# Kernel optimization log

Measured on AMD Instinct MI355X. Metric: run time of the kernel, lower is better.

The kernel has to match this reference:

```python
import jax, jax.numpy as jnp
import numpy as np

B, T, D_IN, H, D_OUT = 64, 512, 256, 1024, 256


def _gru_cell(x, h, Wi, Wh, bi, bh):
    # x: [B, in_dim], h: [B, H]; Wi: [3H, in_dim], Wh: [3H, H]
    gi = x @ Wi.T + bi  # [B, 3H]
    gh = h @ Wh.T + bh  # [B, 3H]
    i_r, i_z, i_n = jnp.split(gi, 3, axis=-1)
    h_r, h_z, h_n = jnp.split(gh, 3, axis=-1)
    r = jax.nn.sigmoid(i_r + h_r)
    z = jax.nn.sigmoid(i_z + h_z)
    n = jnp.tanh(i_n + r * h_n)
    return (1.0 - z) * n + z * h


def setup_inputs() -> dict:
    key = jax.random.key(0)
    ks = jax.random.split(key, 11)
    s_in = 1.0 / np.sqrt(D_IN)
    s_h = 1.0 / np.sqrt(H)
    return {
        "x": jax.random.normal(ks[0], (B, T, D_IN), jnp.float32),
        "Wi0": jax.random.normal(ks[1], (3 * H, D_IN), jnp.float32) * s_in,
        "Wh0": jax.random.normal(ks[2], (3 * H, H), jnp.float32) * s_h,
        "bi0": jax.random.normal(ks[3], (3 * H,), jnp.float32) * s_h,
        "bh0": jax.random.normal(ks[4], (3 * H,), jnp.float32) * s_h,
        "Wi1": jax.random.normal(ks[5], (3 * H, H), jnp.float32) * s_h,
        "Wh1": jax.random.normal(ks[6], (3 * H, H), jnp.float32) * s_h,
        "bi1": jax.random.normal(ks[7], (3 * H,), jnp.float32) * s_h,
        "bh1": jax.random.normal(ks[8], (3 * H,), jnp.float32) * s_h,
        "Wo": jax.random.normal(ks[9], (D_OUT, H), jnp.float32) * s_h,
        "bo": jax.random.normal(ks[10], (D_OUT,), jnp.float32) * s_h,
    }


def reference(x, Wi0, Wh0, bi0, bh0, Wi1, Wh1, bi1, bh1, Wo, bo):
    b = x.shape[0]
    h0 = jnp.zeros((b, H), x.dtype)
    h1 = jnp.zeros((b, H), x.dtype)

    def step(carry, x_t):
        h0, h1 = carry
        h0 = _gru_cell(x_t, h0, Wi0, Wh0, bi0, bh0)
        h1 = _gru_cell(h0, h1, Wi1, Wh1, bi1, bh1)
        return (h0, h1), None

    (h0, h1), _ = jax.lax.scan(step, (h0, h1), jnp.swapaxes(x, 0, 1))
    return h1 @ Wo.T + bo  # [B, D_OUT]
```

## Files before the change

### kernel.cpp

```cpp
#include <hip/hip_runtime.h>

constexpr int kB    = 64;
constexpr int kT    = 512;
constexpr int kDin  = 256;
constexpr int kH    = 1024;
constexpr int kH3   = 3072;
constexpr int kDout = 256;
constexpr int kHB   = kB * kH;

typedef float  f32x4  __attribute__((ext_vector_type(4)));
typedef __bf16 bf16x8 __attribute__((ext_vector_type(8)));
typedef unsigned u32x4 __attribute__((ext_vector_type(4)));
typedef unsigned long long u64;

__device__ __forceinline__ float b2f(unsigned short u) {
  union { float f; unsigned u32; } c; c.u32 = ((unsigned)u) << 16; return c.f;
}
__device__ __forceinline__ unsigned short f2b(float f) {
  union { float f; unsigned u32; } c; c.f = f;
  unsigned r = c.u32 + 0x7fffu + ((c.u32 >> 16) & 1u);
  return (unsigned short)(r >> 16);
}
__device__ __forceinline__ bf16x8 ld8(const unsigned short* p) {
  return *reinterpret_cast<const bf16x8*>(p);
}
__device__ __forceinline__ u64 ald(const u64* p) {
  return __hip_atomic_load(p, __ATOMIC_RELAXED, __HIP_MEMORY_SCOPE_AGENT);
}
__device__ __forceinline__ unsigned ald32(const unsigned* p) {
  return __hip_atomic_load(p, __ATOMIC_RELAXED, __HIP_MEMORY_SCOPE_AGENT);
}
__device__ __forceinline__ void ast32(unsigned* p, unsigned v) {
  __hip_atomic_store(p, v, __ATOMIC_RELAXED, __HIP_MEMORY_SCOPE_AGENT);
}
__device__ __forceinline__ float sigm_(float x) { return 1.f / (1.f + __expf(-x)); }
__device__ __forceinline__ float tanh_(float x) {
  return 1.f - 2.f / (__expf(2.f * x) + 1.f);
}

#define MFMA16(a, b, c) __builtin_amdgcn_mfma_f32_16x16x32_bf16((a), (b), (c), 0, 0, 0)

__device__ __forceinline__ int swzcol(int C, int quad) {
  return (C & ~63) + ((quad ^ (((C >> 3) ^ (C >> 6)) & 7)) << 3);
}

__global__ void gru_prep(const float* __restrict__ x,
                         const float* __restrict__ Wi0, const float* __restrict__ Wh0,
                         const float* __restrict__ bi0, const float* __restrict__ bh0,
                         const float* __restrict__ Wi1, const float* __restrict__ Wh1,
                         const float* __restrict__ bi1, const float* __restrict__ bh1,
                         unsigned short* __restrict__ xb,
                         unsigned short* __restrict__ wi0b, unsigned short* __restrict__ wh0b,
                         unsigned short* __restrict__ wi1b, unsigned short* __restrict__ wh1b,
                         unsigned short* __restrict__ r0, unsigned short* __restrict__ r1,
                         float* __restrict__ bias, unsigned* __restrict__ sync) {
  const int stride = gridDim.x * blockDim.x;
  const int g = blockIdx.x * blockDim.x + threadIdx.x;
  for (int i = g; i < kH3 * kDin; i += stride) wi0b[i] = f2b(Wi0[i]);
  for (int i = g; i < kH3 * kH; i += stride) {
    wh0b[i] = f2b(Wh0[i]); wi1b[i] = f2b(Wi1[i]); wh1b[i] = f2b(Wh1[i]);
  }
  for (int i = g; i < kB * kT * kDin; i += stride) xb[i] = f2b(x[i]);
  for (int i = g; i < kHB; i += stride) { r0[i] = 0; r1[i] = 0; }
  for (int i = g; i < kH; i += stride) {
    bias[0 * kH + i] = bi0[0 * kH + i] + bh0[0 * kH + i];
    bias[1 * kH + i] = bi0[1 * kH + i] + bh0[1 * kH + i];
    bias[2 * kH + i] = bi0[2 * kH + i];
    bias[3 * kH + i] = bh0[2 * kH + i];
    bias[4 * kH + i] = bi1[0 * kH + i] + bh1[0 * kH + i];
    bias[5 * kH + i] = bi1[1 * kH + i] + bh1[1 * kH + i];
    bias[6 * kH + i] = bi1[2 * kH + i];
    bias[7 * kH + i] = bh1[2 * kH + i];
  }
  for (int i = g; i < 1024; i += stride) sync[i] = 0;
}

__global__ void __launch_bounds__(256, 1) gru_main(
    const unsigned short* __restrict__ xb,
    const unsigned short* __restrict__ wi0, const unsigned short* __restrict__ wh0,
    const unsigned short* __restrict__ wi1, const unsigned short* __restrict__ wh1,
    const float* __restrict__ bias,
    unsigned short* __restrict__ r0, unsigned short* __restrict__ r1,
    unsigned* __restrict__ sync, const int rmode,
    const float* __restrict__ Wo, const float* __restrict__ bo,
    float* __restrict__ out) {
  __shared__ unsigned short hl0[16][1032];
  __shared__ unsigned short hl1[16][1032];
  __shared__ float red[2][4][64][5];
  __shared__ bf16x8 wlds[2][32][64];

  const int tid  = threadIdx.x;
  const int lane = tid & 63;
  const int wv   = tid >> 6;
  const int ln15 = lane & 15;
  const int quad = lane >> 4;

  const int xcd   = blockIdx.x & 7;
  const int rest  = blockIdx.x >> 3;
  const int jsub  = rest & 7;
  const int mtile = rest >> 3;
  const int pidx  = xcd * 8 + jsub;

  const int layer = wv >> 1;
  const int kh    = wv & 1;
  const int jrow  = xcd * 128 + jsub * 16 + ln15;
  const int jcol  = jrow;

  const unsigned short *pw_r, *pw_z, *pw_n, *pv_r, *pv_z, *pv_n;
  if (layer == 0) {
    pw_r = wh0 + (size_t)(0 * kH + jrow) * kH + kh * 512 + quad * 8;
    pw_z = wh0 + (size_t)(1 * kH + jrow) * kH + kh * 512 + quad * 8;
    pw_n = wh0 + (size_t)(2 * kH + jrow) * kH + kh * 512 + quad * 8;
    pv_r = wi0 + (size_t)(0 * kH + jrow) * kDin + kh * 128 + quad * 8;
    pv_z = wi0 + (size_t)(1 * kH + jrow) * kDin + kh * 128 + quad * 8;
    pv_n = wi0 + (size_t)(2 * kH + jrow) * kDin + kh * 128 + quad * 8;
  } else {
    pw_r = wh1 + (size_t)(0 * kH + jrow) * kH + kh * 512 + quad * 8;
    pw_z = wh1 + (size_t)(1 * kH + jrow) * kH + kh * 512 + quad * 8;
    pw_n = wh1 + (size_t)(2 * kH + jrow) * kH + kh * 512 + quad * 8;
    pv_r = wi1 + (size_t)(0 * kH + jrow) * kH + kh * 512 + quad * 8;
    pv_z = wi1 + (size_t)(1 * kH + jrow) * kH + kh * 512 + quad * 8;
    pv_n = wi1 + (size_t)(2 * kH + jrow) * kH + kh * 512 + quad * 8;
  }

  const float* bb = bias + layer * 4 * kH;
  const float b_r = bb[jcol];
  const float b_z = bb[kH + jcol];
  const float b_i = bb[2 * kH + jcol];
  const float b_h = bb[3 * kH + jcol];

  bf16x8 W[64];
  if (layer == 0) {
#pragma unroll
    for (int kk = 0; kk < 16; ++kk) {
      W[kk]      = ld8(pw_r + kk * 32);
      W[16 + kk] = ld8(pw_z + kk * 32);
      W[32 + kk] = ld8(pw_n + kk * 32);
    }
#pragma unroll
    for (int kk = 0; kk < 4; ++kk) {
      W[48 + kk] = ld8(pv_r + kk * 32);
      W[52 + kk] = ld8(pv_z + kk * 32);
      W[56 + kk] = ld8(pv_n + kk * 32);
    }
  } else {
#pragma unroll
    for (int kk = 0; kk < 16; ++kk) {
      W[kk]      = ld8(pv_r + kk * 32);
      W[16 + kk] = ld8(pv_z + kk * 32);
      W[32 + kk] = ld8(pv_n + kk * 32);
      W[48 + kk] = ld8(pw_r + kk * 32);
      wlds[kh][kk][lane]      = ld8(pw_z + kk * 32);
      wlds[kh][16 + kk][lane] = ld8(pw_n + kk * 32);
    }
  }

  const f32x4 z4 = {0.f, 0.f, 0.f, 0.f};
  unsigned* fl0 = sync + mtile * 64;
  unsigned* fl1 = sync + 256 + mtile * 64;

  float hprev[4] = {0.f, 0.f, 0.f, 0.f};

  for (int t = 0; t <= kT; ++t) {
    const bool l0c = (t < kT);
    const bool l1c = (t >= 1);
    const int s0r = rmode ? t : (t & 1);
    const int s0w = rmode ? (t + 1) : ((t + 1) & 1);
    const int s1r = rmode ? (t >= 1 ? t - 1 : 0) : ((t >= 1 ? t - 1 : 0) & 1);
    const int s1w = rmode ? t : (t & 1);

    f32x4 a_r = z4, a_z = z4, a_i = z4, a_h = z4;

    if (layer == 0 && l0c) {
      const unsigned short* xp = xb + (size_t)(mtile * 16 + ln15) * (kT * kDin) +
                                 t * kDin + kh * 128 + quad * 8;
      bf16x8 xa[4];
#pragma unroll
      for (int i = 0; i < 4; ++i) xa[i] = ld8(xp + i * 32);
#pragma unroll
      for (int kk = 0; kk < 4; ++kk) {
        a_r = MFMA16(xa[kk], W[48 + kk], a_r);
        a_z = MFMA16(xa[kk], W[52 + kk], a_z);
        a_i = MFMA16(xa[kk], W[56 + kk], a_i);
      }
    }

    if (wv == 0) {
      for (;;) {
        int a = (int)ald32(fl0 + lane);
        int b = (int)ald32(fl1 + lane);
        if (__all(a >= t && b >= t - 1)) break;
        __builtin_amdgcn_s_sleep(4);
      }
    }
    __syncthreads();

    {
      const int r = tid >> 4, s = tid & 15;
      const unsigned short* b0 =
          r0 + (size_t)s0r * kHB + (size_t)(mtile * 16 + r) * kH + s * 64;
      const unsigned short* b1 =
          r1 + (size_t)s1r * kHB + (size_t)(mtile * 16 + r) * kH + s * 64;
      if (rmode) {
        u32x4 d0[8], d1[8];
#pragma unroll
        for (int i = 0; i < 8; ++i) d0[i] = *(const u32x4*)(b0 + i * 8);
#pragma unroll
        for (int i = 0; i < 8; ++i) d1[i] = *(const u32x4*)(b1 + i * 8);
#pragma unroll
        for (int i = 0; i < 8; ++i)
          *(u32x4*)&hl0[r][s * 64 + ((i ^ s) & 7) * 8] = d0[i];
#pragma unroll
        for (int i = 0; i < 8; ++i)
          *(u32x4*)&hl1[r][s * 64 + ((i ^ s) & 7) * 8] = d1[i];
      } else {
        u64 w0[16], w1[16];
#pragma unroll
        for (int i = 0; i < 16; ++i) w0[i] = ald((const u64*)b0 + i);
#pragma unroll
        for (int i = 0; i < 16; ++i) w1[i] = ald((const u64*)b1 + i);
#pragma unroll
        for (int i = 0; i < 16; ++i)
          *(u64*)&hl0[r][s * 64 + (((i >> 1) ^ s) & 7) * 8 + (i & 1) * 4] = w0[i];
#pragma unroll
        for (int i = 0; i < 16; ++i)
          *(u64*)&hl1[r][s * 64 + (((i >> 1) ^ s) & 7) * 8 + (i & 1) * 4] = w1[i];
      }
    }
    __syncthreads();

    const bool active = (layer == 0) ? l0c : l1c;
    if (active) {
      const int kb = kh * 512;
      if (layer == 0) {
#pragma unroll
        for (int kk = 0; kk < 16; ++kk) {
          bf16x8 A = *(const bf16x8*)&hl0[ln15][swzcol(kb + kk * 32, quad)];
          a_r = MFMA16(A, W[kk], a_r);
          a_z = MFMA16(A, W[16 + kk], a_z);
          a_h = MFMA16(A, W[32 + kk], a_h);
        }
      } else {
#pragma unroll
        for (int kk = 0; kk < 16; ++kk) {
          bf16x8 A0 = *(const bf16x8*)&hl0[ln15][swzcol(kb + kk * 32, quad)];
          a_r = MFMA16(A0, W[kk], a_r);
          a_z = MFMA16(A0, W[16 + kk], a_z);
          a_i = MFMA16(A0, W[32 + kk], a_i);
          bf16x8 A1 = *(const bf16x8*)&hl1[ln15][swzcol(kb + kk * 32, quad)];
          a_r = MFMA16(A1, W[48 + kk], a_r);
          a_z = MFMA16(A1, wlds[kh][kk][lane], a_z);
          a_h = MFMA16(A1, wlds[kh][16 + kk][lane], a_h);
        }
      }
    }

    if (((wv == 1) && l0c) || ((wv == 3) && l1c)) {
#pragma unroll
      for (int q = 0; q < 4; ++q) {
        red[layer][0][lane][q] = a_r[q]; red[layer][1][lane][q] = a_z[q];
        red[layer][2][lane][q] = a_i[q]; red[layer][3][lane][q] = a_h[q];
      }
    }
    __syncthreads();

    if (((wv == 0) && l0c) || ((wv == 2) && l1c)) {
      float hv4[4];
#pragma unroll
      for (int q = 0; q < 4; ++q) {
        float sr = a_r[q] + red[layer][0][lane][q];
        float sz = a_z[q] + red[layer][1][lane][q];
        float si = a_i[q] + red[layer][2][lane][q];
        float sh = a_h[q] + red[layer][3][lane][q];
        float rg = sigm_(sr + b_r);
        float zg = sigm_(sz + b_z);
        float ng = tanh_(si + b_i + rg * (sh + b_h));
        hv4[q] = (1.f - zg) * ng + zg * hprev[q];
        hprev[q] = hv4[q];
      }
      unsigned short* dst = (layer == 0) ? r0 + (size_t)s0w * kHB
                                         : r1 + (size_t)s1w * kHB;
#pragma unroll
      for (int q = 0; q < 4; ++q) {
        float pv = __shfl_xor(hv4[q], 1);
        if (!(lane & 1)) {
          unsigned pk = (unsigned)f2b(hv4[q]) | ((unsigned)f2b(pv) << 16);
          unsigned* d = (unsigned*)(dst + (size_t)(mtile * 16 + quad * 4 + q) * kH +
                                    (jcol & ~1));
          ast32(d, pk);
        }
      }
      asm volatile("s_waitcnt vmcnt(0)" ::: "memory");
      if (lane == 0) {
        unsigned* fp = (layer == 0) ? &fl0[pidx] : &fl1[pidx];
        unsigned val = (layer == 0) ? (unsigned)(t + 1) : (unsigned)t;
        ast32(fp, val);
      }
    }
  }

  if (wv == 0) {
    for (;;) {
      int f = (int)ald32(fl1 + lane);
      if (__all(f >= (int)kT)) break;
      __builtin_amdgcn_s_sleep(4);
    }
  }
  __syncthreads();
  {
    const int sfin = rmode ? kT : 0;
    const int r = tid >> 4, s = tid & 15;
    const unsigned short* b1 =
        r1 + (size_t)sfin * kHB + (size_t)(mtile * 16 + r) * kH + s * 64;
    if (rmode) {
      u32x4 d[8];
#pragma unroll
      for (int i = 0; i < 8; ++i) d[i] = *(const u32x4*)(b1 + i * 8);
#pragma unroll
      for (int i = 0; i < 8; ++i) *(u32x4*)&hl0[r][s * 64 + i * 8] = d[i];
    } else {
      u64 w[16];
#pragma unroll
      for (int i = 0; i < 16; ++i) w[i] = ald((const u64*)b1 + i);
#pragma unroll
      for (int i = 0; i < 16; ++i) *(u64*)&hl0[r][s * 64 + i * 4] = w[i];
    }
  }
  __syncthreads();
  {
    const int c  = tid & 31;
    const int rr = tid >> 5;
    const int col = jsub * 32 + c;
    const float* wr = Wo + (size_t)col * kH;
    float acc0 = bo[col], acc1 = bo[col];
#pragma unroll 8
    for (int k = 0; k < kH; k += 4) {
      float4 w4 = *reinterpret_cast<const float4*>(wr + k);
      acc0 += b2f(hl0[rr][k]) * w4.x + b2f(hl0[rr][k + 1]) * w4.y +
              b2f(hl0[rr][k + 2]) * w4.z + b2f(hl0[rr][k + 3]) * w4.w;
      acc1 += b2f(hl0[rr + 8][k]) * w4.x + b2f(hl0[rr + 8][k + 1]) * w4.y +
              b2f(hl0[rr + 8][k + 2]) * w4.z + b2f(hl0[rr + 8][k + 3]) * w4.w;
    }
    out[(mtile * 16 + rr) * kDout + col] = acc0;
    out[(mtile * 16 + rr + 8) * kDout + col] = acc1;
  }
}

extern "C" void kernel_launch(void* const* d_in, const int* in_sizes, int n_in,
                              void* d_out, int out_size, void* d_ws, size_t ws_size,
                              hipStream_t stream) {
  const float* x   = (const float*)d_in[0];
  const float* Wi0 = (const float*)d_in[1];
  const float* Wh0 = (const float*)d_in[2];
  const float* bi0 = (const float*)d_in[3];
  const float* bh0 = (const float*)d_in[4];
  const float* Wi1 = (const float*)d_in[5];
  const float* Wh1 = (const float*)d_in[6];
  const float* bi1 = (const float*)d_in[7];
  const float* bh1 = (const float*)d_in[8];
  const float* Wo  = (const float*)d_in[9];
  const float* bo  = (const float*)d_in[10];

  char* ws = (char*)d_ws;
  size_t off = 0;
  auto take = [&](size_t bytes) {
    size_t r = off;
    off += (bytes + 255) & ~(size_t)255;
    return r;
  };
  unsigned short* xb   = (unsigned short*)(ws + take((size_t)kB * kT * kDin * 2));
  unsigned short* wi0b = (unsigned short*)(ws + take((size_t)kH3 * kDin * 2));
  unsigned short* wh0b = (unsigned short*)(ws + take((size_t)kH3 * kH * 2));
  unsigned short* wi1b = (unsigned short*)(ws + take((size_t)kH3 * kH * 2));
  unsigned short* wh1b = (unsigned short*)(ws + take((size_t)kH3 * kH * 2));
  float*          bias = (float*)(ws + take(8 * kH * sizeof(float)));
  unsigned*       sync = (unsigned*)(ws + take(1024 * sizeof(unsigned)));

  const size_t slot_b = (size_t)kHB * 2;
  int rmode = 1;
  size_t ring_slots = (size_t)kT + 1;
  if (off + 2 * (ring_slots * slot_b) + (1u << 20) > ws_size) {
    rmode = 0;
    ring_slots = 2;
  }
  unsigned short* r0 = (unsigned short*)(ws + take(ring_slots * slot_b));
  unsigned short* r1 = (unsigned short*)(ws + take(ring_slots * slot_b));

  gru_prep<<<2048, 256, 0, stream>>>(x, Wi0, Wh0, bi0, bh0, Wi1, Wh1, bi1, bh1,
                                     xb, wi0b, wh0b, wi1b, wh1b, r0, r1, bias,
                                     sync);
  gru_main<<<256, 256, 0, stream>>>(xb, wi0b, wh0b, wi1b, wh1b, bias, r0, r1,
                                    sync, rmode, Wo, bo, (float*)d_out);
}
```

Measured before the change: 3.381 ms.

## Decouple GRU layer wavepairs with per-pair LDS barriers instead of block-wide syncs

Each layer's wave pair now runs its own time loop with its own global-flag polling, LDS staging buffers and workgroup-scope pair barriers, replacing the lockstep loop that used __syncthreads. Layer 1 stages h0 and computes its input half before waiting for its own previous h1, and half of the hidden-weight tiles move from LDS into registers. Poll sleep is shortened. The aim is to overlap the two layers' critical paths and cut block-wide barrier stalls, at the cost of higher register pressure and spin-wait traffic.

Measured after the change: 3.934 ms. 16.3% more time.

```diff
diff --git a/kernel.cpp b/kernel.cpp
--- a/kernel.cpp
+++ b/kernel.cpp
@@ -42,6 +42,35 @@
 
 __device__ __forceinline__ int swzcol(int C, int quad) {
   return (C & ~63) + ((quad ^ (((C >> 3) ^ (C >> 6)) & 7)) << 3);
+}
+
+__device__ __forceinline__ void stage_seg(unsigned short* ldsrow,
+                                          const unsigned short* src, int s,
+                                          int rmode) {
+  if (rmode) {
+    u32x4 d[8];
+#pragma unroll
+    for (int i = 0; i < 8; ++i) d[i] = *(const u32x4*)(src + i * 8);
+#pragma unroll
+    for (int i = 0; i < 8; ++i)
+      *(u32x4*)&ldsrow[s * 64 + ((i ^ s) & 7) * 8] = d[i];
+  } else {
+    u64 w[16];
+#pragma unroll
+    for (int i = 0; i < 16; ++i) w[i] = ald((const u64*)src + i);
+#pragma unroll
+    for (int i = 0; i < 16; ++i)
+      *(u64*)&ldsrow[s * 64 + (((i >> 1) ^ s) & 7) * 8 + (i & 1) * 4] = w[i];
+  }
+}
+
+__device__ __forceinline__ void pair_bar(unsigned* pb, int me, int other,
+                                         unsigned val, int lane) {
+  if (lane == 0)
+    __hip_atomic_store(&pb[me], val, __ATOMIC_RELEASE,
+                       __HIP_MEMORY_SCOPE_WORKGROUP);
+  while (__hip_atomic_load(&pb[other], __ATOMIC_ACQUIRE,
+                           __HIP_MEMORY_SCOPE_WORKGROUP) < val) {}
 }
 
 __global__ void gru_prep(const float* __restrict__ x,
@@ -84,10 +113,12 @@
     unsigned* __restrict__ sync, const int rmode,
     const float* __restrict__ Wo, const float* __restrict__ bo,
     float* __restrict__ out) {
-  __shared__ unsigned short hl0[16][1032];
-  __shared__ unsigned short hl1[16][1032];
+  __shared__ unsigned short hl0A[16][1032];
+  __shared__ unsigned short hl0B[16][1032];
+  __shared__ unsigned short hl1v[16][1032];
   __shared__ float red[2][4][64][5];
-  __shared__ bf16x8 wlds[2][32][64];
+  __shared__ bf16x8 wlds[2][16][64];
+  __shared__ unsigned pbar[4];
 
   const int tid  = threadIdx.x;
   const int lane = tid & 63;
@@ -129,7 +160,7 @@
   const float b_i = bb[2 * kH + jcol];
   const float b_h = bb[3 * kH + jcol];
 
-  bf16x8 W[64];
+  bf16x8 W[64], W2[16];
   if (layer == 0) {
 #pragma unroll
     for (int kk = 0; kk < 16; ++kk) {
@@ -150,10 +181,13 @@
       W[16 + kk] = ld8(pv_z + kk * 32);
       W[32 + kk] = ld8(pv_n + kk * 32);
       W[48 + kk] = ld8(pw_r + kk * 32);
-      wlds[kh][kk][lane]      = ld8(pw_z + kk * 32);
-      wlds[kh][16 + kk][lane] = ld8(pw_n + kk * 32);
-    }
-  }
+      W2[kk]     = ld8(pw_z + kk * 32);
+      wlds[kh][kk][lane] = ld8(pw_n + kk * 32);
+    }
+  }
+
+  if (tid < 4) pbar[tid] = 0;
+  __syncthreads();
 
   const f32x4 z4 = {0.f, 0.f, 0.f, 0.f};
   unsigned* fl0 = sync + mtile * 64;
@@ -161,150 +195,190 @@
 
   float hprev[4] = {0.f, 0.f, 0.f, 0.f};
 
-  for (int t = 0; t <= kT; ++t) {
-    const bool l0c = (t < kT);
-    const bool l1c = (t >= 1);
-    const int s0r = rmode ? t : (t & 1);
-    const int s0w = rmode ? (t + 1) : ((t + 1) & 1);
-    const int s1r = rmode ? (t >= 1 ? t - 1 : 0) : ((t >= 1 ? t - 1 : 0) & 1);
-    const int s1w = rmode ? t : (t & 1);
-
-    f32x4 a_r = z4, a_z = z4, a_i = z4, a_h = z4;
-
-    if (layer == 0 && l0c) {
-      const unsigned short* xp = xb + (size_t)(mtile * 16 + ln15) * (kT * kDin) +
-                                 t * kDin + kh * 128 + quad * 8;
-      bf16x8 xa[4];
-#pragma unroll
-      for (int i = 0; i < 4; ++i) xa[i] = ld8(xp + i * 32);
-#pragma unroll
-      for (int kk = 0; kk < 4; ++kk) {
-        a_r = MFMA16(xa[kk], W[48 + kk], a_r);
-        a_z = MFMA16(xa[kk], W[52 + kk], a_z);
-        a_i = MFMA16(xa[kk], W[56 + kk], a_i);
-      }
-    }
-
-    if (wv == 0) {
+  if (layer == 0) {
+    const int p    = tid;
+    const int srow = p >> 3;
+    const int sseg = p & 7;
+    for (int t = 0; t < kT; ++t) {
+      const int s0r = rmode ? t : (t & 1);
+      const int s0w = rmode ? (t + 1) : ((t + 1) & 1);
+      f32x4 a_r = z4, a_z = z4, a_i = z4, a_h = z4;
+
+      {
+        const unsigned short* xp = xb + (size_t)(mtile * 16 + ln15) * (kT * kDin) +
+                                   t * kDin + kh * 128 + quad * 8;
+        bf16x8 xa[4];
+#pragma unroll
+        for (int i = 0; i < 4; ++i) xa[i] = ld8(xp + i * 32);
+#pragma unroll
+        for (int kk = 0; kk < 4; ++kk) {
+          a_r = MFMA16(xa[kk], W[48 + kk], a_r);
+          a_z = MFMA16(xa[kk], W[52 + kk], a_z);
+          a_i = MFMA16(xa[kk], W[56 + kk], a_i);
+        }
+      }
+
       for (;;) {
         int a = (int)ald32(fl0 + lane);
+        bool ok;
+        if (rmode) ok = __all(a >= t);
+        else { int b = (int)ald32(fl1 + lane); ok = __all(a >= t && b >= t - 1); }
+        if (ok) break;
+        __builtin_amdgcn_s_sleep(1);
+      }
+
+      {
+        const unsigned short* rb =
+            r0 + (size_t)s0r * kHB + (size_t)(mtile * 16 + srow) * kH;
+        stage_seg(hl0A[srow], rb + sseg * 64, sseg, rmode);
+        stage_seg(hl0A[srow], rb + (sseg + 8) * 64, sseg + 8, rmode);
+      }
+      pair_bar(pbar, wv, wv ^ 1, 2u * t + 1, lane);
+
+      const int kb = kh * 512;
+#pragma unroll
+      for (int kk = 0; kk < 16; ++kk) {
+        bf16x8 A = *(const bf16x8*)&hl0A[ln15][swzcol(kb + kk * 32, quad)];
+        a_r = MFMA16(A, W[kk], a_r);
+        a_z = MFMA16(A, W[16 + kk], a_z);
+        a_h = MFMA16(A, W[32 + kk], a_h);
+      }
+
+      if (wv == 1) {
+#pragma unroll
+        for (int q = 0; q < 4; ++q) {
+          red[0][0][lane][q] = a_r[q]; red[0][1][lane][q] = a_z[q];
+          red[0][2][lane][q] = a_i[q]; red[0][3][lane][q] = a_h[q];
+        }
+      }
+      pair_bar(pbar, wv, wv ^ 1, 2u * t + 2, lane);
+
+      if (wv == 0) {
+        float hv4[4];
+#pragma unroll
+        for (int q = 0; q < 4; ++q) {
+          float s_r = a_r[q] + red[0][0][lane][q];
+          float s_z = a_z[q] + red[0][1][lane][q];
+          float s_i = a_i[q] + red[0][2][lane][q];
+          float s_h = a_h[q] + red[0][3][lane][q];
+          float rg = sigm_(s_r + b_r);
+          float zg = sigm_(s_z + b_z);
+          float ng = tanh_(s_i + b_i + rg * (s_h + b_h));
+          hv4[q] = (1.f - zg) * ng + zg * hprev[q];
+          hprev[q] = hv4[q];
+        }
+        unsigned short* dst = r0 + (size_t)s0w * kHB;
+#pragma unroll
+        for (int q = 0; q < 4; ++q) {
+          float pv = __shfl_xor(hv4[q], 1);
+          if (!(lane & 1)) {
+            unsigned pk = (unsigned)f2b(hv4[q]) | ((unsigned)f2b(pv) << 16);
+            ast32((unsigned*)(dst + (size_t)(mtile * 16 + quad * 4 + q) * kH +
+                              (jcol & ~1)),
+                  pk);
+          }
+        }
+        asm volatile("s_waitcnt vmcnt(0)" ::: "memory");
+        if (lane == 0) ast32(&fl0[pidx], (unsigned)(t + 1));
+      }
+    }
+  } else {
+    const int p    = tid - 128;
+    const int srow = p >> 3;
+    const int sseg = p & 7;
+    for (int t = 1; t <= kT; ++t) {
+      const int s0r = rmode ? t : (t & 1);
+      const int s1r = rmode ? (t - 1) : ((t - 1) & 1);
+      const int s1w = rmode ? t : (t & 1);
+
+      for (;;) {
+        int a = (int)ald32(fl0 + lane);
+        if (__all(a >= t)) break;
+        __builtin_amdgcn_s_sleep(1);
+      }
+      {
+        const unsigned short* rb =
+            r0 + (size_t)s0r * kHB + (size_t)(mtile * 16 + srow) * kH;
+        stage_seg(hl0B[srow], rb + sseg * 64, sseg, rmode);
+        stage_seg(hl0B[srow], rb + (sseg + 8) * 64, sseg + 8, rmode);
+      }
+      pair_bar(pbar, wv, wv ^ 1, 3u * (t - 1) + 1, lane);
+
+      f32x4 a_r = z4, a_z = z4, a_i = z4, a_h = z4;
+      const int kb = kh * 512;
+#pragma unroll
+      for (int kk = 0; kk < 16; ++kk) {
+        bf16x8 A0 = *(const bf16x8*)&hl0B[ln15][swzcol(kb + kk * 32, quad)];
+        a_r = MFMA16(A0, W[kk], a_r);
+        a_z = MFMA16(A0, W[16 + kk], a_z);
+        a_i = MFMA16(A0, W[32 + kk], a_i);
+      }
+
+      for (;;) {
         int b = (int)ald32(fl1 + lane);
-        if (__all(a >= t && b >= t - 1)) break;
-        __builtin_amdgcn_s_sleep(4);
-      }
-    }
-    __syncthreads();
-
-    {
-      const int r = tid >> 4, s = tid & 15;
-      const unsigned short* b0 =
-          r0 + (size_t)s0r * kHB + (size_t)(mtile * 16 + r) * kH + s * 64;
-      const unsigned short* b1 =
-          r1 + (size_t)s1r * kHB + (size_t)(mtile * 16 + r) * kH + s * 64;
-      if (rmode) {
-        u32x4 d0[8], d1[8];
-#pragma unroll
-        for (int i = 0; i < 8; ++i) d0[i] = *(const u32x4*)(b0 + i * 8);
-#pragma unroll
-        for (int i = 0; i < 8; ++i) d1[i] = *(const u32x4*)(b1 + i * 8);
-#pragma unroll
-        for (int i = 0; i < 8; ++i)
-          *(u32x4*)&hl0[r][s * 64 + ((i ^ s) & 7) * 8] = d0[i];
-#pragma unroll
-        for (int i = 0; i < 8; ++i)
-          *(u32x4*)&hl1[r][s * 64 + ((i ^ s) & 7) * 8] = d1[i];
-      } else {
-        u64 w0[16], w1[16];
-#pragma unroll
-        for (int i = 0; i < 16; ++i) w0[i] = ald((const u64*)b0 + i);
-#pragma unroll
-        for (int i = 0; i < 16; ++i) w1[i] = ald((const u64*)b1 + i);
-#pragma unroll
-        for (int i = 0; i < 16; ++i)
-          *(u64*)&hl0[r][s * 64 + (((i >> 1) ^ s) & 7) * 8 + (i & 1) * 4] = w0[i];
-#pragma unroll
-        for (int i = 0; i < 16; ++i)
-          *(u64*)&hl1[r][s * 64 + (((i >> 1) ^ s) & 7) * 8 + (i & 1) * 4] = w1[i];
-      }
-    }
-    __syncthreads();
-
-    const bool active = (layer == 0) ? l0c : l1c;
-    if (active) {
-      const int kb = kh * 512;
-      if (layer == 0) {
-#pragma unroll
-        for (int kk = 0; kk < 16; ++kk) {
-          bf16x8 A = *(const bf16x8*)&hl0[ln15][swzcol(kb + kk * 32, quad)];
-          a_r = MFMA16(A, W[kk], a_r);
-          a_z = MFMA16(A, W[16 + kk], a_z);
-          a_h = MFMA16(A, W[32 + kk], a_h);
-        }
-      } else {
-#pragma unroll
-        for (int kk = 0; kk < 16; ++kk) {
-          bf16x8 A0 = *(const bf16x8*)&hl0[ln15][swzcol(kb + kk * 32, quad)];
-          a_r = MFMA16(A0, W[kk], a_r);
-          a_z = MFMA16(A0, W[16 + kk], a_z);
-          a_i = MFMA16(A0, W[32 + kk], a_i);
-          bf16x8 A1 = *(const bf16x8*)&hl1[ln15][swzcol(kb + kk * 32, quad)];
-          a_r = MFMA16(A1, W[48 + kk], a_r);
-          a_z = MFMA16(A1, wlds[kh][kk][lane], a_z);
-          a_h = MFMA16(A1, wlds[kh][16 + kk][lane], a_h);
-        }
-      }
-    }
-
-    if (((wv == 1) && l0c) || ((wv == 3) && l1c)) {
-#pragma unroll
-      for (int q = 0; q < 4; ++q) {
-        red[layer][0][lane][q] = a_r[q]; red[layer][1][lane][q] = a_z[q];
-        red[layer][2][lane][q] = a_i[q]; red[layer][3][lane][q] = a_h[q];
-      }
-    }
-    __syncthreads();
-
-    if (((wv == 0) && l0c) || ((wv == 2) && l1c)) {
-      float hv4[4];
-#pragma unroll
-      for (int q = 0; q < 4; ++q) {
-        float sr = a_r[q] + red[layer][0][lane][q];
-        float sz = a_z[q] + red[layer][1][lane][q];
-        float si = a_i[q] + red[layer][2][lane][q];
-        float sh = a_h[q] + red[layer][3][lane][q];
-        float rg = sigm_(sr + b_r);
-        float zg = sigm_(sz + b_z);
-        float ng = tanh_(si + b_i + rg * (sh + b_h));
-        hv4[q] = (1.f - zg) * ng + zg * hprev[q];
-        hprev[q] = hv4[q];
-      }
-      unsigned short* dst = (layer == 0) ? r0 + (size_t)s0w * kHB
-                                         : r1 + (size_t)s1w * kHB;
-#pragma unroll
-      for (int q = 0; q < 4; ++q) {
-        float pv = __shfl_xor(hv4[q], 1);
-        if (!(lane & 1)) {
-          unsigned pk = (unsigned)f2b(hv4[q]) | ((unsigned)f2b(pv) << 16);
-          unsigned* d = (unsigned*)(dst + (size_t)(mtile * 16 + quad * 4 + q) * kH +
-                                    (jcol & ~1));
-          ast32(d, pk);
-        }
-      }
-      asm volatile("s_waitcnt vmcnt(0)" ::: "memory");
-      if (lane == 0) {
-        unsigned* fp = (layer == 0) ? &fl0[pidx] : &fl1[pidx];
-        unsigned val = (layer == 0) ? (unsigned)(t + 1) : (unsigned)t;
-        ast32(fp, val);
-      }
-    }
-  }
-
-  if (wv == 0) {
-    for (;;) {
-      int f = (int)ald32(fl1 + lane);
-      if (__all(f >= (int)kT)) break;
-      __builtin_amdgcn_s_sleep(4);
-    }
+        if (__all(b >= t - 1)) break;
+        __builtin_amdgcn_s_sleep(1);
+      }
+      {
+        const unsigned short* rb =
+            r1 + (size_t)s1r * kHB + (size_t)(mtile * 16 + srow) * kH;
+        stage_seg(hl1v[srow], rb + sseg * 64, sseg, rmode);
+        stage_seg(hl1v[srow], rb + (sseg + 8) * 64, sseg + 8, rmode);
+      }
+      pair_bar(pbar, wv, wv ^ 1, 3u * (t - 1) + 2, lane);
+
+#pragma unroll
+      for (int kk = 0; kk < 16; ++kk) {
+        bf16x8 A1 = *(const bf16x8*)&hl1v[ln15][swzcol(kb + kk * 32, quad)];
+        a_r = MFMA16(A1, W[48 + kk], a_r);
+        a_z = MFMA16(A1, W2[kk], a_z);
+        a_h = MFMA16(A1, wlds[kh][kk][lane], a_h);
+      }
+
+      if (wv == 3) {
+#pragma unroll
+        for (int q = 0; q < 4; ++q) {
+          red[1][0][lane][q] = a_r[q]; red[1][1][lane][q] = a_z[q];
+          red[1][2][lane][q] = a_i[q]; red[1][3][lane][q] = a_h[q];
+        }
+      }
+      pair_bar(pbar, wv, wv ^ 1, 3u * (t - 1) + 3, lane);
+
+      if (wv == 2) {
+        float hv4[4];
+#pragma unroll
+        for (int q = 0; q < 4; ++q) {
+          float s_r = a_r[q] + red[1][0][lane][q];
+          float s_z = a_z[q] + red[1][1][lane][q];
+          float s_i = a_i[q] + red[1][2][lane][q];
+          float s_h = a_h[q] + red[1][3][lane][q];
+          float rg = sigm_(s_r + b_r);
+          float zg = sigm_(s_z + b_z);
+          float ng = tanh_(s_i + b_i + rg * (s_h + b_h));
+          hv4[q] = (1.f - zg) * ng + zg * hprev[q];
+          hprev[q] = hv4[q];
+        }
+        unsigned short* dst = r1 + (size_t)s1w * kHB;
+#pragma unroll
+        for (int q = 0; q < 4; ++q) {
+          float pv = __shfl_xor(hv4[q], 1);
+          if (!(lane & 1)) {
+            unsigned pk = (unsigned)f2b(hv4[q]) | ((unsigned)f2b(pv) << 16);
+            ast32((unsigned*)(dst + (size_t)(mtile * 16 + quad * 4 + q) * kH +
+                              (jcol & ~1)),
+                  pk);
+          }
+        }
+        asm volatile("s_waitcnt vmcnt(0)" ::: "memory");
+        if (lane == 0) ast32(&fl1[pidx], (unsigned)t);
+      }
+    }
+  }
+
+  for (;;) {
+    int f = (int)ald32(fl1 + lane);
+    if (__all(f >= (int)kT)) break;
+    __builtin_amdgcn_s_sleep(1);
   }
   __syncthreads();
   {
@@ -317,13 +391,13 @@
 #pragma unroll
       for (int i = 0; i < 8; ++i) d[i] = *(const u32x4*)(b1 + i * 8);
 #pragma unroll
-      for (int i = 0; i < 8; ++i) *(u32x4*)&hl0[r][s * 64 + i * 8] = d[i];
+      for (int i = 0; i < 8; ++i) *(u32x4*)&hl0A[r][s * 64 + i * 8] = d[i];
     } else {
       u64 w[16];
 #pragma unroll
       for (int i = 0; i < 16; ++i) w[i] = ald((const u64*)b1 + i);
 #pragma unroll
-      for (int i = 0; i < 16; ++i) *(u64*)&hl0[r][s * 64 + i * 4] = w[i];
+      for (int i = 0; i < 16; ++i) *(u64*)&hl0A[r][s * 64 + i * 4] = w[i];
     }
   }
   __syncthreads();
@@ -336,10 +410,10 @@
 #pragma unroll 8
     for (int k = 0; k < kH; k += 4) {
       float4 w4 = *reinterpret_cast<const float4*>(wr + k);
-      acc0 += b2f(hl0[rr][k]) * w4.x + b2f(hl0[rr][k + 1]) * w4.y +
-              b2f(hl0[rr][k + 2]) * w4.z + b2f(hl0[rr][k + 3]) * w4.w;
-      acc1 += b2f(hl0[rr + 8][k]) * w4.x + b2f(hl0[rr + 8][k + 1]) * w4.y +
-              b2f(hl0[rr + 8][k + 2]) * w4.z + b2f(hl0[rr + 8][k + 3]) * w4.w;
+      acc0 += b2f(hl0A[rr][k]) * w4.x + b2f(hl0A[rr][k + 1]) * w4.y +
+              b2f(hl0A[rr][k + 2]) * w4.z + b2f(hl0A[rr][k + 3]) * w4.w;
+      acc1 += b2f(hl0A[rr + 8][k]) * w4.x + b2f(hl0A[rr + 8][k + 1]) * w4.y +
+              b2f(hl0A[rr + 8][k + 2]) * w4.z + b2f(hl0A[rr + 8][k + 3]) * w4.w;
     }
     out[(mtile * 16 + rr) * kDout + col] = acc0;
     out[(mtile * 16 + rr + 8) * kDout + col] = acc1;
```
